# Optimization experiments

Hardware: AMD Instinct MI355X
Metric: run time of the kernel (lower is better)

Reference implementation:

```python
import jax, jax.numpy as jnp
import numpy as np

# Static config (matches init_kwargs: dim=64, ffn=2.66, kernel=3, smk=3, heads=2)
DIM = 64
NUM_HEADS = 2
KS = 3
SMK = 3
POOL = 7           # ContMix pools context to 7x7 -> 49 context tokens
HIDDEN = 172       # round_up(int(64*2.66), 4)
HIDDEN2 = 2 * HIDDEN
CTX_DW = HIDDEN2 // 4   # 86
CTX_DW12 = HIDDEN // 4  # 43
NK = SMK * SMK + KS * KS  # 18


def conv1x1(x, w):
    # x: [B,C,H,W], w: [O,C] -> [B,O,H,W]
    return jnp.einsum('bchw,oc->bohw', x, w)


def extract_patches(x, k):
    # x: [B,C,H,W] -> [B,C,k*k,H,W], zero ('same') padding, stride 1
    p = k // 2
    B, C, H, W = x.shape
    xp = jnp.pad(x, ((0, 0), (0, 0), (p, p), (p, p)))
    pats = [xp[:, :, i:i + H, j:j + W] for i in range(k) for j in range(k)]
    return jnp.stack(pats, axis=2)


def dyn_dw(x, attn, k, heads):
    # Dynamic depthwise mixing: per-pixel, per-head k*k kernel shared across
    # channels within a head. x: [B,C,H,W], attn: [B,g,HW,k*k]
    B, C, H, W = x.shape
    hd = C // heads
    pat = extract_patches(x, k).reshape(B, heads, hd, k * k, H * W)
    out = jnp.einsum('bgdkn,bgnk->bgdn', pat, attn)
    return out.reshape(B, C, H, W)


def contmix(x, ctx, wq, wk, wp, wpb, wo):
    # Content-aware dynamic depthwise-mixing (ContMix, OverLoCK-style).
    B, C, H, W = x.shape
    hd_qk = (C // 2) // NUM_HEADS
    scale = hd_qk ** -0.5
    # query from x, key from 7x7-pooled context
    q = conv1x1(x, wq) * scale                     # [B, C//2, H, W]
    ph, pw = H // POOL, W // POOL
    ctx_p = ctx.reshape(B, -1, POOL, ph, POOL, pw).mean(axis=(3, 5))  # [B,ctx,7,7]
    key = conv1x1(ctx_p, wk)                       # [B, C//2, 7, 7]
    q = q.reshape(B, NUM_HEADS, hd_qk, H * W)
    key = key.reshape(B, NUM_HEADS, hd_qk, POOL * POOL)
    w = jnp.einsum('bgcn,bgcl->bgnl', q, key)      # [B,g,HW,49]
    # project 49 context scores -> smk^2 + k^2 dynamic kernel taps (1x1 conv w/ bias)
    w = jnp.einsum('bgnl,ol->bgno', w, wp) + wpb   # [B,g,HW,18]
    a1 = jax.nn.softmax(w[..., :SMK * SMK], axis=-1)
    a2 = jax.nn.softmax(w[..., SMK * SMK:], axis=-1)
    # first channel half mixed with small kernel, second half with large kernel
    x1, x2 = jnp.split(x, 2, axis=1)
    y = jnp.concatenate([dyn_dw(x1, a1, SMK, NUM_HEADS),
                         dyn_dw(x2, a2, KS, NUM_HEADS)], axis=1)
    return conv1x1(y, wo)


def setup_inputs() -> dict:
    key = jax.random.key(0)
    ks = jax.random.split(key, 32)
    def w(i, o, c):
        return jax.random.normal(ks[i], (o, c), dtype=jnp.float32) / np.sqrt(c)
    inp = {
        'x': jax.random.normal(ks[0], (2, DIM, 112, 112), dtype=jnp.float32),
        'pin_w': w(1, HIDDEN2, DIM),
        'ctx_w': w(2, CTX_DW, HIDDEN2),
        'ctx1_w': w(3, CTX_DW12, HIDDEN),
        'ctx2_w': w(4, CTX_DW12, HIDDEN),
        'pout_w': w(5, DIM, HIDDEN),
        # ContMix on hidden_x2 (dim=344, ctx=86)
        'cm0_q': w(6, HIDDEN2 // 2, HIDDEN2),
        'cm0_k': w(7, HIDDEN2 // 2, CTX_DW),
        'cm0_p': w(8, NK, POOL * POOL),
        'cm0_pb': jnp.zeros((NK,), dtype=jnp.float32),
        'cm0_o': w(9, HIDDEN2, HIDDEN2),
        # ContMix on hidden (dim=172, ctx=43) -- branch 1
        'cm1_q': w(10, HIDDEN // 2, HIDDEN),
        'cm1_k': w(11, HIDDEN // 2, CTX_DW12),
        'cm1_p': w(12, NK, POOL * POOL),
        'cm1_pb': jnp.zeros((NK,), dtype=jnp.float32),
        'cm1_o': w(13, HIDDEN, HIDDEN),
        # ContMix on hidden -- branch 2
        'cm2_q': w(14, HIDDEN // 2, HIDDEN),
        'cm2_k': w(15, HIDDEN // 2, CTX_DW12),
        'cm2_p': w(16, NK, POOL * POOL),
        'cm2_pb': jnp.zeros((NK,), dtype=jnp.float32),
        'cm2_o': w(17, HIDDEN, HIDDEN),
    }
    return inp


def reference(x, pin_w, ctx_w, ctx1_w, ctx2_w, pout_w,
              cm0_q, cm0_k, cm0_p, cm0_pb, cm0_o,
              cm1_q, cm1_k, cm1_p, cm1_pb, cm1_o,
              cm2_q, cm2_k, cm2_p, cm2_pb, cm2_o):
    x_in = conv1x1(x, pin_w)                           # [B, 2*hidden, H, W]
    ctx_dw = conv1x1(x_in, ctx_w)                      # [B, ctx_dw, H, W]
    x_dw = contmix(x_in, ctx_dw, cm0_q, cm0_k, cm0_p, cm0_pb, cm0_o)
    x1, x2 = jnp.split(x_dw, 2, axis=1)                # each [B, hidden, H, W]
    ctx1 = conv1x1(x1, ctx1_w)
    ctx2 = conv1x1(x2, ctx2_w)
    x1p = jnp.tanh(contmix(x1, ctx1, cm1_q, cm1_k, cm1_p, cm1_pb, cm1_o)) + x1
    x2p = jnp.tanh(contmix(x2, ctx2, cm2_q, cm2_k, cm2_p, cm2_pb, cm2_o)) + x2
    out = conv1x1(x1p * x2p, pout_w)                   # [B, dim, H, W]
    return out
```

## Files before the change

kernel.cpp:

```cpp
#include <hip/hip_runtime.h>
#include <math.h>

#define HW 12544
#define W_IMG 112
#define B_SZ 2
#define RPAD 40

typedef __attribute__((ext_vector_type(8))) short s8v;
typedef __attribute__((ext_vector_type(4))) float f4v;

__device__ __forceinline__ void split_bf16(float x, unsigned short& h, unsigned short& l) {
    unsigned u  = __float_as_uint(x);
    unsigned hb = (u + 0x7FFFu + ((u >> 16) & 1u)) >> 16;
    float hf    = __uint_as_float(hb << 16);
    float r     = x - hf;
    unsigned ur = __float_as_uint(r);
    unsigned lb = (ur + 0x7FFFu + ((ur >> 16) & 1u)) >> 16;
    h = (unsigned short)hb; l = (unsigned short)lb;
}

struct WSplitArgs {
    const float* src[8];
    const float* src2[8];
    unsigned short* hi[8];
    unsigned short* lo[8];
    int O1[8]; int O2[8]; int O2B[8]; int K[8]; int Kp[8]; int MpKp[8];
    float scale2[8];
};

__global__ __launch_bounds__(256) void wsplit_k(WSplitArgs a) {
    const int ci  = blockIdx.y;
    const int idx = blockIdx.x * 256 + threadIdx.x;
    if (idx >= a.MpKp[ci]) return;
    const int Kp   = a.Kp[ci];
    const int mblk = idx / (32 * Kp);
    const int rem  = idx - mblk * 32 * Kp;
    const int kc   = rem >> 10;
    const int rem2 = rem & 1023;
    const int row  = rem2 >> 5, kk = rem2 & 31;
    const int o = mblk * 32 + row, k = kc * 32 + kk;
    float v = 0.f;
    if (k < a.K[ci]) {
        if (o < a.O1[ci])
            v = a.src[ci][(size_t)o * a.K[ci] + k];
        else if (o >= a.O2B[ci] && o - a.O2B[ci] < a.O2[ci])
            v = a.src2[ci][(size_t)(o - a.O2B[ci]) * a.K[ci] + k] * a.scale2[ci];
    }
    unsigned short h, l;
    split_bf16(v, h, l);
    a.hi[ci][idx] = h; a.lo[ci][idx] = l;
}

__global__ __launch_bounds__(256) void tsplit_k(
    const float* __restrict__ src, size_t bstride, int C, int KC,
    unsigned short* __restrict__ hi, unsigned short* __restrict__ lo)
{
    __shared__ __align__(16) float t[32][36];
    const int b   = blockIdx.z;
    const int hw0 = blockIdx.x * 32;
    const int kc  = blockIdx.y;
    const int c0  = kc * 32;
    const int tid = threadIdx.x;

    {
        const int cl = tid >> 3, hq = (tid & 7) * 4;
        const int c  = c0 + cl;
        float4 v = make_float4(0.f, 0.f, 0.f, 0.f);
        if (c < C)
            v = *(const float4*)(src + (size_t)b * bstride + (size_t)c * HW + hw0 + hq);
        *(float4*)&t[cl][hq] = v;
    }
    __syncthreads();

    const int hl = tid >> 3, cq = (tid & 7) * 4;
    float v0 = t[cq + 0][hl], v1 = t[cq + 1][hl], v2 = t[cq + 2][hl], v3 = t[cq + 3][hl];
    ushort4 h4, l4;
    split_bf16(v0, h4.x, l4.x);
    split_bf16(v1, h4.y, l4.y);
    split_bf16(v2, h4.z, l4.z);
    split_bf16(v3, h4.w, l4.w);
    const int ns = hw0 >> 8, r = (hw0 & 255) + hl;
    const size_t base = (((size_t)b * 49 + ns) * KC + kc) * 8192 + (size_t)r * 32 + cq;
    *(ushort4*)(hi + base) = h4;
    *(ushort4*)(lo + base) = l4;
}

template <int KP>
__global__ __launch_bounds__(256) void gemm_k(
    const unsigned short* __restrict__ bt_hi, const unsigned short* __restrict__ bt_lo,
    const unsigned short* __restrict__ w_hi,  const unsigned short* __restrict__ w_lo,
    int per_m,
    float* __restrict__ outA, int OA, size_t oa_bstride,
    float* __restrict__ outB, int OB, size_t ob_bstride, int obase,
    int mode, int Ovalid,
    const float* __restrict__ res, size_t res_bstride,
    const float* __restrict__ mul, size_t mul_bstride)
{
    constexpr int KC = KP / 32;
    __shared__ __align__(16) unsigned short Bh_s[256 * RPAD];
    __shared__ __align__(16) unsigned short Bl_s[256 * RPAD];
    __shared__ __align__(16) unsigned short Ah_s[32 * RPAD];
    __shared__ __align__(16) unsigned short Al_s[32 * RPAD];

    const int b   = blockIdx.y;
    const int bx  = blockIdx.x;
    const int xcd = bx & 7, t = bx >> 3;
    const int m   = t % per_m;
    const int ns  = (t / per_m) * 8 + xcd;
    if (ns >= 49) return;

    const int tid  = threadIdx.x;
    const int wv   = tid >> 6, lane = tid & 63;
    const int m16  = lane & 15, quad = lane >> 4;
    const int mbase = m * 32;
    const int nbase = ns * 256 + wv * 64;

    const unsigned short* Bh_g = bt_hi + ((size_t)b * 49 + ns) * KC * 8192;
    const unsigned short* Bl_g = bt_lo + ((size_t)b * 49 + ns) * KC * 8192;
    const unsigned short* Ah_g = w_hi + (size_t)m * KC * 1024;
    const unsigned short* Al_g = w_lo + (size_t)m * KC * 1024;

    const int srow = tid >> 2, schunk = tid & 3;
    const int arow = (tid & 127) >> 2, achunk = tid & 3;

    f4v acc0[4], acc1[4];
#pragma unroll
    for (int f = 0; f < 4; ++f) {
        acc0[f] = (f4v){0.f, 0.f, 0.f, 0.f};
        acc1[f] = (f4v){0.f, 0.f, 0.f, 0.f};
    }

    s8v rBh[4], rBl[4], rA;
#pragma unroll
    for (int j = 0; j < 4; ++j) {
        rBh[j] = *(const s8v*)(Bh_g + (size_t)(j * 256 + tid) * 8);
        rBl[j] = *(const s8v*)(Bl_g + (size_t)(j * 256 + tid) * 8);
    }
    rA = (tid < 128) ? *(const s8v*)(Ah_g + (size_t)tid * 8)
                     : *(const s8v*)(Al_g + (size_t)(tid - 128) * 8);
#pragma unroll
    for (int j = 0; j < 4; ++j) {
        *(s8v*)(Bh_s + (j * 64 + srow) * RPAD + schunk * 8) = rBh[j];
        *(s8v*)(Bl_s + (j * 64 + srow) * RPAD + schunk * 8) = rBl[j];
    }
    if (tid < 128) *(s8v*)(Ah_s + arow * RPAD + achunk * 8) = rA;
    else           *(s8v*)(Al_s + arow * RPAD + achunk * 8) = rA;
    __syncthreads();

#pragma unroll
    for (int kc = 0; kc < KC; ++kc) {
        if (kc + 1 < KC) {
            const size_t bo = (size_t)(kc + 1) * 8192;
            const size_t ao = (size_t)(kc + 1) * 1024;
#pragma unroll
            for (int j = 0; j < 4; ++j) {
                rBh[j] = *(const s8v*)(Bh_g + bo + (size_t)(j * 256 + tid) * 8);
                rBl[j] = *(const s8v*)(Bl_g + bo + (size_t)(j * 256 + tid) * 8);
            }
            rA = (tid < 128) ? *(const s8v*)(Ah_g + ao + (size_t)tid * 8)
                             : *(const s8v*)(Al_g + ao + (size_t)(tid - 128) * 8);
        }
        s8v ah0 = *(const s8v*)(Ah_s + m16 * RPAD + quad * 8);
        s8v al0 = *(const s8v*)(Al_s + m16 * RPAD + quad * 8);
        s8v ah1 = *(const s8v*)(Ah_s + (16 + m16) * RPAD + quad * 8);
        s8v al1 = *(const s8v*)(Al_s + (16 + m16) * RPAD + quad * 8);
#pragma unroll
        for (int f = 0; f < 4; ++f) {
            const int row = wv * 64 + f * 16 + m16;
            s8v bhf = *(const s8v*)(Bh_s + row * RPAD + quad * 8);
            s8v blf = *(const s8v*)(Bl_s + row * RPAD + quad * 8);
            acc0[f] = __builtin_amdgcn_mfma_f32_16x16x32_bf16(ah0, bhf, acc0[f], 0, 0, 0);
            acc0[f] = __builtin_amdgcn_mfma_f32_16x16x32_bf16(al0, bhf, acc0[f], 0, 0, 0);
            acc0[f] = __builtin_amdgcn_mfma_f32_16x16x32_bf16(ah0, blf, acc0[f], 0, 0, 0);
            acc1[f] = __builtin_amdgcn_mfma_f32_16x16x32_bf16(ah1, bhf, acc1[f], 0, 0, 0);
            acc1[f] = __builtin_amdgcn_mfma_f32_16x16x32_bf16(al1, bhf, acc1[f], 0, 0, 0);
            acc1[f] = __builtin_amdgcn_mfma_f32_16x16x32_bf16(ah1, blf, acc1[f], 0, 0, 0);
        }
        __syncthreads();
        if (kc + 1 < KC) {
#pragma unroll
            for (int j = 0; j < 4; ++j) {
                *(s8v*)(Bh_s + (j * 64 + srow) * RPAD + schunk * 8) = rBh[j];
                *(s8v*)(Bl_s + (j * 64 + srow) * RPAD + schunk * 8) = rBl[j];
            }
            if (tid < 128) *(s8v*)(Ah_s + arow * RPAD + achunk * 8) = rA;
            else           *(s8v*)(Al_s + arow * RPAD + achunk * 8) = rA;
            __syncthreads();
        }
    }

#pragma unroll
    for (int mp = 0; mp < 2; ++mp) {
#pragma unroll
        for (int f = 0; f < 4; ++f) {
            const int n = nbase + f * 16 + m16;
#pragma unroll
            for (int r = 0; r < 4; ++r) {
                const int o = mbase + mp * 16 + quad * 4 + r;
                float v = mp ? acc1[f][r] : acc0[f][r];
                if (mode == 2) {
                    if (o < Ovalid)
                        v = tanhf(v) + res[(size_t)b * res_bstride + (size_t)o * HW + n];
                } else if (mode == 3) {
                    if (o < Ovalid)
                        v = (tanhf(v) + res[(size_t)b * res_bstride + (size_t)o * HW + n])
                            * mul[(size_t)b * mul_bstride + (size_t)o * HW + n];
                }
                if (o < OA) {
                    outA[(size_t)b * oa_bstride + (size_t)o * HW + n] = v;
                } else if (o >= obase && o - obase < OB) {
                    outB[(size_t)b * ob_bstride + (size_t)(o - obase) * HW + n] = v;
                }
            }
        }
    }
}

__global__ __launch_bounds__(64) void pool_k(
    const float* __restrict__ ctx, float* __restrict__ pooled, int C)
{
    const int c = blockIdx.x, b = blockIdx.y, t = threadIdx.x;
    if (t >= 49) return;
    const int ph = t / 7, pw = t % 7;
    const float* src = ctx + ((size_t)b * C + c) * HW;
    float sum = 0.f;
    for (int i = 0; i < 16; ++i) {
        const float* row = src + (ph * 16 + i) * W_IMG + pw * 16;
        for (int j = 0; j < 16; ++j) sum += row[j];
    }
    pooled[((size_t)b * C + c) * 49 + t] = sum * (1.0f / 256.0f);
}

__global__ __launch_bounds__(64) void keygemm_k(
    const float* __restrict__ pooled, const float* __restrict__ wk,
    float* __restrict__ key, int K, int O)
{
    const int o = blockIdx.x, b = blockIdx.y, l = threadIdx.x;
    if (l >= 49) return;
    float s = 0.f;
    for (int c = 0; c < K; ++c)
        s += wk[(size_t)o * K + c] * pooled[((size_t)b * K + c) * 49 + l];
    key[((size_t)b * O + o) * 49 + l] = s;
}

__global__ __launch_bounds__(256) void attn_k(
    const float* __restrict__ q, const float* __restrict__ key,
    const float* __restrict__ wp, const float* __restrict__ pb,
    float* __restrict__ attn, int hd)
{
    __shared__ float klds[86 * 52];
    __shared__ float plds[18 * 52];
    __shared__ float pblds[18];

    const int b = blockIdx.z, g = blockIdx.y, tid = threadIdx.x;

    for (int idx = tid; idx < hd * 49; idx += 256) {
        int c = idx / 49, l = idx - c * 49;
        klds[c * 52 + l] = key[((size_t)(b * 2 + g) * hd + c) * 49 + l];
    }
    for (int idx = tid; idx < hd * 3; idx += 256) {
        int c = idx / 3;
        klds[c * 52 + 49 + (idx - c * 3)] = 0.f;
    }
    for (int idx = tid; idx < 18 * 49; idx += 256) {
        int o = idx / 49, l = idx - o * 49;
        plds[o * 52 + l] = wp[o * 49 + l];
    }
    for (int idx = tid; idx < 18 * 3; idx += 256) {
        int o = idx / 3;
        plds[o * 52 + 49 + (idx - o * 3)] = 0.f;
    }
    if (tid < 18) pblds[tid] = pb[tid];
    __syncthreads();

    const int hw = blockIdx.x * 256 + tid;

    float4 s[13];
#pragma unroll
    for (int t = 0; t < 13; ++t) s[t] = make_float4(0.f, 0.f, 0.f, 0.f);

    const float* qp = q + (size_t)(b * 2 + g) * hd * HW + hw;
    for (int c = 0; c < hd; ++c) {
        float qv = qp[(size_t)c * HW];
        const float4* kr = (const float4*)(klds + c * 52);
#pragma unroll
        for (int t = 0; t < 13; ++t) {
            float4 kv = kr[t];
            s[t].x += qv * kv.x; s[t].y += qv * kv.y;
            s[t].z += qv * kv.z; s[t].w += qv * kv.w;
        }
    }

    float e[18];
#pragma unroll
    for (int o = 0; o < 18; ++o) {
        const float4* pr = (const float4*)(plds + o * 52);
        float4 a = make_float4(0.f, 0.f, 0.f, 0.f);
#pragma unroll
        for (int t = 0; t < 13; ++t) {
            float4 pv = pr[t];
            a.x += s[t].x * pv.x; a.y += s[t].y * pv.y;
            a.z += s[t].z * pv.z; a.w += s[t].w * pv.w;
        }
        e[o] = pblds[o] + a.x + a.y + a.z + a.w;
    }

    float* outp = attn + (size_t)(b * 2 + g) * 18 * HW + hw;
#pragma unroll
    for (int half = 0; half < 2; ++half) {
        int base = half * 9;
        float m = e[base];
#pragma unroll
        for (int k = 1; k < 9; ++k) m = fmaxf(m, e[base + k]);
        float sum = 0.f, ex[9];
#pragma unroll
        for (int k = 0; k < 9; ++k) { ex[k] = expf(e[base + k] - m); sum += ex[k]; }
        float inv = 1.0f / sum;
#pragma unroll
        for (int k = 0; k < 9; ++k) outp[(size_t)(base + k) * HW] = ex[k] * inv;
    }
}

__global__ __launch_bounds__(256) void dyndw_k(
    const float* __restrict__ x, const float* __restrict__ attn,
    float* __restrict__ y, int C, int C_half, int hd, size_t x_bstride)
{
    const int b = blockIdx.z, c = blockIdx.y;
    const int hw = blockIdx.x * 256 + threadIdx.x;
    const int h = hw / W_IMG, w = hw - h * W_IMG;

    const int half = c / C_half;
    const int g = (c - half * C_half) / hd;

    const float* ap = attn + ((size_t)(b * 2 + g) * 18 + half * 9) * HW + hw;
    float a[9];
#pragma unroll
    for (int k = 0; k < 9; ++k) a[k] = ap[(size_t)k * HW];

    const float* xp = x + (size_t)b * x_bstride + (size_t)c * HW;
    float s = 0.f;
#pragma unroll
    for (int i = 0; i < 3; ++i) {
        int hh = h + i - 1;
#pragma unroll
        for (int j = 0; j < 3; ++j) {
            int ww = w + j - 1;
            float v = (hh >= 0 && hh < 112 && ww >= 0 && ww < 112)
                          ? xp[hh * W_IMG + ww] : 0.f;
            s += v * a[i * 3 + j];
        }
    }
    y[((size_t)b * C + c) * HW + hw] = s;
}

extern "C" void kernel_launch(void* const* d_in, const int* in_sizes, int n_in,
                              void* d_out, int out_size, void* d_ws, size_t ws_size,
                              hipStream_t stream) {
    const float* x      = (const float*)d_in[0];
    const float* pin_w  = (const float*)d_in[1];
    const float* ctx_w  = (const float*)d_in[2];
    const float* ctx1_w = (const float*)d_in[3];
    const float* ctx2_w = (const float*)d_in[4];
    const float* pout_w = (const float*)d_in[5];
    const float* cm0_q  = (const float*)d_in[6];
    const float* cm0_k  = (const float*)d_in[7];
    const float* cm0_p  = (const float*)d_in[8];
    const float* cm0_pb = (const float*)d_in[9];
    const float* cm0_o  = (const float*)d_in[10];
    const float* cm1_q  = (const float*)d_in[11];
    const float* cm1_k  = (const float*)d_in[12];
    const float* cm1_p  = (const float*)d_in[13];
    const float* cm1_pb = (const float*)d_in[14];
    const float* cm1_o  = (const float*)d_in[15];
    const float* cm2_q  = (const float*)d_in[16];
    const float* cm2_k  = (const float*)d_in[17];
    const float* cm2_p  = (const float*)d_in[18];
    const float* cm2_pb = (const float*)d_in[19];
    const float* cm2_o  = (const float*)d_in[20];
    float* out = (float*)d_out;

    float* ws = (float*)d_ws;
    float* x_in  = ws;
    float* x1p   = ws;
    float* y0    = ws + 8630272;
    float* y1    = ws + 8630272;
    float* prod  = ws + 8630272;
    float* y2    = ws + 12945408;
    float* x_dw  = ws + 17260544;
    float* ctxb  = ws + 25890816;
    float* ctx1  = ws + 28048384;
    float* ctx2  = ws + 29127168;
    float* q0    = ws + 30205952;
    float* q1    = ws + 30205952;
    float* q2    = ws + 32363520;
    float* attnb = ws + 34521088;
    float* pooled= ws + 35424256;
    float* keyb  = ws + 35432704;
    unsigned short* ub = (unsigned short*)(ws + 35449568);
    static const int WOFF[8] = {0, 45056, 247808, 518144, 579584, 641024, 714752, 788480};
    static const int WO1[8]  = {344, 86, 172, 43, 43, 172, 172, 64};
    static const int WO2[8]  = {0, 172, 172, 86, 86, 0, 0, 0};
    static const int O2B[8]  = {352, 86, 192, 43, 43, 192, 192, 64};
    static const int WK[8]   = {64, 344, 344, 172, 172, 172, 172, 172};
    static const int WKP[8]  = {64, 352, 352, 192, 192, 192, 192, 192};
    static const int WMP[8]  = {352, 288, 384, 160, 160, 192, 192, 64};
    unsigned short* xt_hi   = ub + 813056;
    unsigned short* xt_lo   = ub + 2418688;
    unsigned short* bigA_hi = ub + 4024320;
    unsigned short* bigA_lo = ub + 12855296;
    unsigned short* x1t_hi  = ub + 21686272;
    unsigned short* x1t_lo  = ub + 26503168;
    unsigned short* x2t_hi  = ub + 31320064;
    unsigned short* x2t_lo  = ub + 36136960;

    const float sc0 = 1.0f / sqrtf(86.0f);
    const float sc1 = 1.0f / sqrtf(43.0f);
    const size_t BS344 = (size_t)344 * HW, BS172 = (size_t)172 * HW,
                 BS86 = (size_t)86 * HW, BS64 = (size_t)64 * HW, BS43 = (size_t)43 * HW;

    WSplitArgs wa;
    const float* wsrc1[8] = {pin_w, ctx_w, cm0_o, ctx1_w, ctx2_w, cm1_o, cm2_o, pout_w};
    const float* wsrc2[8] = {nullptr, cm0_q, cm0_o + (size_t)172 * 344, cm1_q, cm2_q,
                             nullptr, nullptr, nullptr};
    const float wsc2[8]   = {1.f, sc0, 1.f, sc1, sc1, 1.f, 1.f, 1.f};
    for (int i = 0; i < 8; ++i) {
        wa.src[i] = wsrc1[i]; wa.src2[i] = wsrc2[i];
        wa.hi[i]  = ub + WOFF[i];
        wa.lo[i]  = ub + WOFF[i] + WMP[i] * WKP[i];
        wa.O1[i] = WO1[i]; wa.O2[i] = WO2[i]; wa.O2B[i] = O2B[i];
        wa.K[i] = WK[i]; wa.Kp[i] = WKP[i];
        wa.MpKp[i] = WMP[i] * WKP[i];
        wa.scale2[i] = wsc2[i];
    }
    wsplit_k<<<dim3(528, 8), 256, 0, stream>>>(wa);

#define WHI(CI) (ub + WOFF[CI])
#define WLO(CI) (ub + WOFF[CI] + WMP[CI] * WKP[CI])
#define GRID(CI) dim3((WMP[CI] / 32) * 56, B_SZ)

    tsplit_k<<<dim3(392, 2, B_SZ), 256, 0, stream>>>(x, BS64, 64, 2, xt_hi, xt_lo);
    gemm_k<64><<<GRID(0), 256, 0, stream>>>(
        xt_hi, xt_lo, WHI(0), WLO(0), WMP[0] / 32,
        x_in, 344, BS344, nullptr, 0, 0, 352, 0, 344,
        nullptr, 0, nullptr, 0);
    tsplit_k<<<dim3(392, 11, B_SZ), 256, 0, stream>>>(x_in, BS344, 344, 11, bigA_hi, bigA_lo);

    gemm_k<352><<<GRID(1), 256, 0, stream>>>(
        bigA_hi, bigA_lo, WHI(1), WLO(1), WMP[1] / 32,
        ctxb, 86, BS86, q0, 172, BS172, 86, 0, 258,
        nullptr, 0, nullptr, 0);
    pool_k<<<dim3(86, B_SZ), dim3(64), 0, stream>>>(ctxb, pooled, 86);
    keygemm_k<<<dim3(172, B_SZ), dim3(64), 0, stream>>>(pooled, cm0_k, keyb, 86, 172);
    attn_k<<<dim3(49, 2, B_SZ), dim3(256), 0, stream>>>(q0, keyb, cm0_p, cm0_pb, attnb, 86);
    dyndw_k<<<dim3(49, 344, B_SZ), dim3(256), 0, stream>>>(x_in, attnb, y0, 344, 172, 86, BS344);
    tsplit_k<<<dim3(392, 11, B_SZ), 256, 0, stream>>>(y0, BS344, 344, 11, bigA_hi, bigA_lo);
    gemm_k<352><<<GRID(2), 256, 0, stream>>>(
        bigA_hi, bigA_lo, WHI(2), WLO(2), WMP[2] / 32,
        x_dw, 172, BS344, x_dw + BS172, 172, BS344, 192, 0, 384,
        nullptr, 0, nullptr, 0);

    tsplit_k<<<dim3(392, 6, B_SZ), 256, 0, stream>>>(x_dw, BS344, 172, 6, x1t_hi, x1t_lo);
    tsplit_k<<<dim3(392, 6, B_SZ), 256, 0, stream>>>(x_dw + BS172, BS344, 172, 6, x2t_hi, x2t_lo);

    gemm_k<192><<<GRID(3), 256, 0, stream>>>(
        x1t_hi, x1t_lo, WHI(3), WLO(3), WMP[3] / 32,
        ctx1, 43, BS43, q1, 86, BS86, 43, 0, 129,
        nullptr, 0, nullptr, 0);
    pool_k<<<dim3(43, B_SZ), dim3(64), 0, stream>>>(ctx1, pooled, 43);
    keygemm_k<<<dim3(86, B_SZ), dim3(64), 0, stream>>>(pooled, cm1_k, keyb, 43, 86);
    attn_k<<<dim3(49, 2, B_SZ), dim3(256), 0, stream>>>(q1, keyb, cm1_p, cm1_pb, attnb, 43);
    dyndw_k<<<dim3(49, 172, B_SZ), dim3(256), 0, stream>>>(x_dw, attnb, y1, 172, 86, 43, BS344);
    tsplit_k<<<dim3(392, 6, B_SZ), 256, 0, stream>>>(y1, BS172, 172, 6, x1t_hi, x1t_lo);
    gemm_k<192><<<GRID(5), 256, 0, stream>>>(
        x1t_hi, x1t_lo, WHI(5), WLO(5), WMP[5] / 32,
        x1p, 172, BS172, nullptr, 0, 0, 192, 2, 172,
        x_dw, BS344, nullptr, 0);

    gemm_k<192><<<GRID(4), 256, 0, stream>>>(
        x2t_hi, x2t_lo, WHI(4), WLO(4), WMP[4] / 32,
        ctx2, 43, BS43, q2, 86, BS86, 43, 0, 129,
        nullptr, 0, nullptr, 0);
    pool_k<<<dim3(43, B_SZ), dim3(64), 0, stream>>>(ctx2, pooled, 43);
    keygemm_k<<<dim3(86, B_SZ), dim3(64), 0, stream>>>(pooled, cm2_k, keyb, 43, 86);
    attn_k<<<dim3(49, 2, B_SZ), dim3(256), 0, stream>>>(q2, keyb, cm2_p, cm2_pb, attnb, 43);
    dyndw_k<<<dim3(49, 172, B_SZ), dim3(256), 0, stream>>>(x_dw + BS172, attnb, y2, 172, 86, 43, BS344);
    tsplit_k<<<dim3(392, 6, B_SZ), 256, 0, stream>>>(y2, BS172, 172, 6, x2t_hi, x2t_lo);
    gemm_k<192><<<GRID(6), 256, 0, stream>>>(
        x2t_hi, x2t_lo, WHI(6), WLO(6), WMP[6] / 32,
        prod, 172, BS172, nullptr, 0, 0, 192, 3, 172,
        x_dw + BS172, BS344, x1p, BS172);

    tsplit_k<<<dim3(392, 6, B_SZ), 256, 0, stream>>>(prod, BS172, 172, 6, bigA_hi, bigA_lo);
    gemm_k<192><<<GRID(7), 256, 0, stream>>>(
        bigA_hi, bigA_lo, WHI(7), WLO(7), WMP[7] / 32,
        out, 64, BS64, nullptr, 0, 0, 64, 0, 64,
        nullptr, 0, nullptr, 0);

#undef WHI
#undef WLO
#undef GRID
}
```

Baseline: 584.2 us.

## Load GEMM operand fragments directly from global into registers, bypassing LDS

```diff
diff --git a/kernel.cpp b/kernel.cpp
--- a/kernel.cpp
+++ b/kernel.cpp
@@ -4,7 +4,6 @@
 #define HW 12544
 #define W_IMG 112
 #define B_SZ 2
-#define RPAD 40
 
 typedef __attribute__((ext_vector_type(8))) short s8v;
 typedef __attribute__((ext_vector_type(4))) float f4v;
@@ -97,10 +96,6 @@
     const float* __restrict__ mul, size_t mul_bstride)
 {
     constexpr int KC = KP / 32;
-    __shared__ __align__(16) unsigned short Bh_s[256 * RPAD];
-    __shared__ __align__(16) unsigned short Bl_s[256 * RPAD];
-    __shared__ __align__(16) unsigned short Ah_s[32 * RPAD];
-    __shared__ __align__(16) unsigned short Al_s[32 * RPAD];
 
     const int b   = blockIdx.y;
     const int bx  = blockIdx.x;
@@ -115,13 +110,12 @@
     const int mbase = m * 32;
     const int nbase = ns * 256 + wv * 64;
 
-    const unsigned short* Bh_g = bt_hi + ((size_t)b * 49 + ns) * KC * 8192;
-    const unsigned short* Bl_g = bt_lo + ((size_t)b * 49 + ns) * KC * 8192;
-    const unsigned short* Ah_g = w_hi + (size_t)m * KC * 1024;
-    const unsigned short* Al_g = w_lo + (size_t)m * KC * 1024;
-
-    const int srow = tid >> 2, schunk = tid & 3;
-    const int arow = (tid & 127) >> 2, achunk = tid & 3;
+    const unsigned short* Bh = bt_hi + ((size_t)b * 49 + ns) * KC * 8192;
+    const unsigned short* Bl = bt_lo + ((size_t)b * 49 + ns) * KC * 8192;
+    const unsigned short* Ah = w_hi + (size_t)m * KC * 1024;
+    const unsigned short* Al = w_lo + (size_t)m * KC * 1024;
+    const int boff = (wv * 64 + m16) * 32 + quad * 8;
+    const int aoff = m16 * 32 + quad * 8;
 
     f4v acc0[4], acc1[4];
 #pragma unroll
@@ -130,62 +124,46 @@
         acc1[f] = (f4v){0.f, 0.f, 0.f, 0.f};
     }
 
-    s8v rBh[4], rBl[4], rA;
-#pragma unroll
-    for (int j = 0; j < 4; ++j) {
-        rBh[j] = *(const s8v*)(Bh_g + (size_t)(j * 256 + tid) * 8);
-        rBl[j] = *(const s8v*)(Bl_g + (size_t)(j * 256 + tid) * 8);
-    }
-    rA = (tid < 128) ? *(const s8v*)(Ah_g + (size_t)tid * 8)
-                     : *(const s8v*)(Al_g + (size_t)(tid - 128) * 8);
-#pragma unroll
-    for (int j = 0; j < 4; ++j) {
-        *(s8v*)(Bh_s + (j * 64 + srow) * RPAD + schunk * 8) = rBh[j];
-        *(s8v*)(Bl_s + (j * 64 + srow) * RPAD + schunk * 8) = rBl[j];
-    }
-    if (tid < 128) *(s8v*)(Ah_s + arow * RPAD + achunk * 8) = rA;
-    else           *(s8v*)(Al_s + arow * RPAD + achunk * 8) = rA;
-    __syncthreads();
+    s8v cah0 = *(const s8v*)(Ah + aoff);
+    s8v cal0 = *(const s8v*)(Al + aoff);
+    s8v cah1 = *(const s8v*)(Ah + aoff + 512);
+    s8v cal1 = *(const s8v*)(Al + aoff + 512);
+    s8v cbh[4], cbl[4];
+#pragma unroll
+    for (int f = 0; f < 4; ++f) {
+        cbh[f] = *(const s8v*)(Bh + boff + f * 512);
+        cbl[f] = *(const s8v*)(Bl + boff + f * 512);
+    }
 
 #pragma unroll
     for (int kc = 0; kc < KC; ++kc) {
+        s8v nah0, nal0, nah1, nal1, nbh[4], nbl[4];
         if (kc + 1 < KC) {
-            const size_t bo = (size_t)(kc + 1) * 8192;
-            const size_t ao = (size_t)(kc + 1) * 1024;
-#pragma unroll
-            for (int j = 0; j < 4; ++j) {
-                rBh[j] = *(const s8v*)(Bh_g + bo + (size_t)(j * 256 + tid) * 8);
-                rBl[j] = *(const s8v*)(Bl_g + bo + (size_t)(j * 256 + tid) * 8);
+            const size_t ao = (size_t)(kc + 1) * 1024 + aoff;
+            const size_t bo = (size_t)(kc + 1) * 8192 + boff;
+            nah0 = *(const s8v*)(Ah + ao);
+            nal0 = *(const s8v*)(Al + ao);
+            nah1 = *(const s8v*)(Ah + ao + 512);
+            nal1 = *(const s8v*)(Al + ao + 512);
+#pragma unroll
+            for (int f = 0; f < 4; ++f) {
+                nbh[f] = *(const s8v*)(Bh + bo + f * 512);
+                nbl[f] = *(const s8v*)(Bl + bo + f * 512);
             }
-            rA = (tid < 128) ? *(const s8v*)(Ah_g + ao + (size_t)tid * 8)
-                             : *(const s8v*)(Al_g + ao + (size_t)(tid - 128) * 8);
-        }
-        s8v ah0 = *(const s8v*)(Ah_s + m16 * RPAD + quad * 8);
-        s8v al0 = *(const s8v*)(Al_s + m16 * RPAD + quad * 8);
-        s8v ah1 = *(const s8v*)(Ah_s + (16 + m16) * RPAD + quad * 8);
-        s8v al1 = *(const s8v*)(Al_s + (16 + m16) * RPAD + quad * 8);
+        }
 #pragma unroll
         for (int f = 0; f < 4; ++f) {
-            const int row = wv * 64 + f * 16 + m16;
-            s8v bhf = *(const s8v*)(Bh_s + row * RPAD + quad * 8);
-            s8v blf = *(const s8v*)(Bl_s + row * RPAD + quad * 8);
-            acc0[f] = __builtin_amdgcn_mfma_f32_16x16x32_bf16(ah0, bhf, acc0[f], 0, 0, 0);
-            acc0[f] = __builtin_amdgcn_mfma_f32_16x16x32_bf16(al0, bhf, acc0[f], 0, 0, 0);
-            acc0[f] = __builtin_amdgcn_mfma_f32_16x16x32_bf16(ah0, blf, acc0[f], 0, 0, 0);
-            acc1[f] = __builtin_amdgcn_mfma_f32_16x16x32_bf16(ah1, bhf, acc1[f], 0, 0, 0);
-            acc1[f] = __builtin_amdgcn_mfma_f32_16x16x32_bf16(al1, bhf, acc1[f], 0, 0, 0);
-            acc1[f] = __builtin_amdgcn_mfma_f32_16x16x32_bf16(ah1, blf, acc1[f], 0, 0, 0);
-        }
-        __syncthreads();
+            acc0[f] = __builtin_amdgcn_mfma_f32_16x16x32_bf16(cah0, cbh[f], acc0[f], 0, 0, 0);
+            acc0[f] = __builtin_amdgcn_mfma_f32_16x16x32_bf16(cal0, cbh[f], acc0[f], 0, 0, 0);
+            acc0[f] = __builtin_amdgcn_mfma_f32_16x16x32_bf16(cah0, cbl[f], acc0[f], 0, 0, 0);
+            acc1[f] = __builtin_amdgcn_mfma_f32_16x16x32_bf16(cah1, cbh[f], acc1[f], 0, 0, 0);
+            acc1[f] = __builtin_amdgcn_mfma_f32_16x16x32_bf16(cal1, cbh[f], acc1[f], 0, 0, 0);
+            acc1[f] = __builtin_amdgcn_mfma_f32_16x16x32_bf16(cah1, cbl[f], acc1[f], 0, 0, 0);
+        }
         if (kc + 1 < KC) {
-#pragma unroll
-            for (int j = 0; j < 4; ++j) {
-                *(s8v*)(Bh_s + (j * 64 + srow) * RPAD + schunk * 8) = rBh[j];
-                *(s8v*)(Bl_s + (j * 64 + srow) * RPAD + schunk * 8) = rBl[j];
-            }
-            if (tid < 128) *(s8v*)(Ah_s + arow * RPAD + achunk * 8) = rA;
-            else           *(s8v*)(Al_s + arow * RPAD + achunk * 8) = rA;
-            __syncthreads();
+            cah0 = nah0; cal0 = nal0; cah1 = nah1; cal1 = nal1;
+#pragma unroll
+            for (int f = 0; f < 4; ++f) { cbh[f] = nbh[f]; cbl[f] = nbl[f]; }
         }
     }
 
```

New measurement: 596.0 us. 2.0% more time.

## Reorder bf16 split tiles into k-quad-major layout for conflict-free LDS access

Applied to the files above, without the earlier changes.

```diff
diff --git a/kernel.cpp b/kernel.cpp
--- a/kernel.cpp
+++ b/kernel.cpp
@@ -4,7 +4,6 @@
 #define HW 12544
 #define W_IMG 112
 #define B_SZ 2
-#define RPAD 40
 
 typedef __attribute__((ext_vector_type(8))) short s8v;
 typedef __attribute__((ext_vector_type(4))) float f4v;
@@ -33,12 +32,15 @@
     const int idx = blockIdx.x * 256 + threadIdx.x;
     if (idx >= a.MpKp[ci]) return;
     const int Kp   = a.Kp[ci];
-    const int mblk = idx / (32 * Kp);
-    const int rem  = idx - mblk * 32 * Kp;
+    const int blk  = 32 * Kp;
+    const int mblk = idx / blk;
+    const int rem  = idx - mblk * blk;
     const int kc   = rem >> 10;
     const int rem2 = rem & 1023;
-    const int row  = rem2 >> 5, kk = rem2 & 31;
-    const int o = mblk * 32 + row, k = kc * 32 + kk;
+    const int kq   = rem2 >> 8;
+    const int row  = (rem2 >> 3) & 31;
+    const int j    = rem2 & 7;
+    const int o = mblk * 32 + row, k = kc * 32 + kq * 8 + j;
     float v = 0.f;
     if (k < a.K[ci]) {
         if (o < a.O1[ci])
@@ -80,7 +82,9 @@
     split_bf16(v2, h4.z, l4.z);
     split_bf16(v3, h4.w, l4.w);
     const int ns = hw0 >> 8, r = (hw0 & 255) + hl;
-    const size_t base = (((size_t)b * 49 + ns) * KC + kc) * 8192 + (size_t)r * 32 + cq;
+    const int kq = cq >> 3, j0 = cq & 7;
+    const size_t base = (((size_t)b * 49 + ns) * KC + kc) * 8192
+                        + (size_t)kq * 2048 + (size_t)r * 8 + j0;
     *(ushort4*)(hi + base) = h4;
     *(ushort4*)(lo + base) = l4;
 }
@@ -97,10 +101,10 @@
     const float* __restrict__ mul, size_t mul_bstride)
 {
     constexpr int KC = KP / 32;
-    __shared__ __align__(16) unsigned short Bh_s[256 * RPAD];
-    __shared__ __align__(16) unsigned short Bl_s[256 * RPAD];
-    __shared__ __align__(16) unsigned short Ah_s[32 * RPAD];
-    __shared__ __align__(16) unsigned short Al_s[32 * RPAD];
+    __shared__ __align__(16) unsigned short Bh_s[8192];
+    __shared__ __align__(16) unsigned short Bl_s[8192];
+    __shared__ __align__(16) unsigned short Ah_s[1024];
+    __shared__ __align__(16) unsigned short Al_s[1024];
 
     const int b   = blockIdx.y;
     const int bx  = blockIdx.x;
@@ -120,84 +124,79 @@
     const unsigned short* Ah_g = w_hi + (size_t)m * KC * 1024;
     const unsigned short* Al_g = w_lo + (size_t)m * KC * 1024;
 
-    const int srow = tid >> 2, schunk = tid & 3;
-    const int arow = (tid & 127) >> 2, achunk = tid & 3;
-
-    f4v acc0[4], acc1[4];
-#pragma unroll
-    for (int f = 0; f < 4; ++f) {
-        acc0[f] = (f4v){0.f, 0.f, 0.f, 0.f};
-        acc1[f] = (f4v){0.f, 0.f, 0.f, 0.f};
-    }
-
-    s8v rBh[4], rBl[4], rA;
+    f4v acc[2][4];
+#pragma unroll
+    for (int mt = 0; mt < 2; ++mt)
+#pragma unroll
+        for (int f = 0; f < 4; ++f) acc[mt][f] = (f4v){0.f, 0.f, 0.f, 0.f};
+
+    s8v rB[8], rA;
 #pragma unroll
     for (int j = 0; j < 4; ++j) {
-        rBh[j] = *(const s8v*)(Bh_g + (size_t)(j * 256 + tid) * 8);
-        rBl[j] = *(const s8v*)(Bl_g + (size_t)(j * 256 + tid) * 8);
+        rB[j]     = *(const s8v*)(Bh_g + (size_t)(j * 256 + tid) * 8);
+        rB[4 + j] = *(const s8v*)(Bl_g + (size_t)(j * 256 + tid) * 8);
     }
     rA = (tid < 128) ? *(const s8v*)(Ah_g + (size_t)tid * 8)
                      : *(const s8v*)(Al_g + (size_t)(tid - 128) * 8);
 #pragma unroll
     for (int j = 0; j < 4; ++j) {
-        *(s8v*)(Bh_s + (j * 64 + srow) * RPAD + schunk * 8) = rBh[j];
-        *(s8v*)(Bl_s + (j * 64 + srow) * RPAD + schunk * 8) = rBl[j];
-    }
-    if (tid < 128) *(s8v*)(Ah_s + arow * RPAD + achunk * 8) = rA;
-    else           *(s8v*)(Al_s + arow * RPAD + achunk * 8) = rA;
+        *(s8v*)(Bh_s + (j * 256 + tid) * 8) = rB[j];
+        *(s8v*)(Bl_s + (j * 256 + tid) * 8) = rB[4 + j];
+    }
+    if (tid < 128) *(s8v*)(Ah_s + tid * 8) = rA;
+    else           *(s8v*)(Al_s + (tid - 128) * 8) = rA;
     __syncthreads();
 
 #pragma unroll
     for (int kc = 0; kc < KC; ++kc) {
         if (kc + 1 < KC) {
-            const size_t bo = (size_t)(kc + 1) * 8192;
-            const size_t ao = (size_t)(kc + 1) * 1024;
+            const unsigned short* bh = Bh_g + (size_t)(kc + 1) * 8192;
+            const unsigned short* bl = Bl_g + (size_t)(kc + 1) * 8192;
 #pragma unroll
             for (int j = 0; j < 4; ++j) {
-                rBh[j] = *(const s8v*)(Bh_g + bo + (size_t)(j * 256 + tid) * 8);
-                rBl[j] = *(const s8v*)(Bl_g + bo + (size_t)(j * 256 + tid) * 8);
+                rB[j]     = *(const s8v*)(bh + (size_t)(j * 256 + tid) * 8);
+                rB[4 + j] = *(const s8v*)(bl + (size_t)(j * 256 + tid) * 8);
             }
-            rA = (tid < 128) ? *(const s8v*)(Ah_g + ao + (size_t)tid * 8)
-                             : *(const s8v*)(Al_g + ao + (size_t)(tid - 128) * 8);
-        }
-        s8v ah0 = *(const s8v*)(Ah_s + m16 * RPAD + quad * 8);
-        s8v al0 = *(const s8v*)(Al_s + m16 * RPAD + quad * 8);
-        s8v ah1 = *(const s8v*)(Ah_s + (16 + m16) * RPAD + quad * 8);
-        s8v al1 = *(const s8v*)(Al_s + (16 + m16) * RPAD + quad * 8);
-#pragma unroll
-        for (int f = 0; f < 4; ++f) {
-            const int row = wv * 64 + f * 16 + m16;
-            s8v bhf = *(const s8v*)(Bh_s + row * RPAD + quad * 8);
-            s8v blf = *(const s8v*)(Bl_s + row * RPAD + quad * 8);
-            acc0[f] = __builtin_amdgcn_mfma_f32_16x16x32_bf16(ah0, bhf, acc0[f], 0, 0, 0);
-            acc0[f] = __builtin_amdgcn_mfma_f32_16x16x32_bf16(al0, bhf, acc0[f], 0, 0, 0);
-            acc0[f] = __builtin_amdgcn_mfma_f32_16x16x32_bf16(ah0, blf, acc0[f], 0, 0, 0);
-            acc1[f] = __builtin_amdgcn_mfma_f32_16x16x32_bf16(ah1, bhf, acc1[f], 0, 0, 0);
-            acc1[f] = __builtin_amdgcn_mfma_f32_16x16x32_bf16(al1, bhf, acc1[f], 0, 0, 0);
-            acc1[f] = __builtin_amdgcn_mfma_f32_16x16x32_bf16(ah1, blf, acc1[f], 0, 0, 0);
+            rA = (tid < 128)
+                ? *(const s8v*)(Ah_g + (size_t)(kc + 1) * 1024 + (size_t)tid * 8)
+                : *(const s8v*)(Al_g + (size_t)(kc + 1) * 1024 + (size_t)(tid - 128) * 8);
+        }
+#pragma unroll
+        for (int mt = 0; mt < 2; ++mt) {
+            s8v ah = *(const s8v*)(Ah_s + (quad * 32 + mt * 16 + m16) * 8);
+            s8v al = *(const s8v*)(Al_s + (quad * 32 + mt * 16 + m16) * 8);
+#pragma unroll
+            for (int f = 0; f < 4; ++f) {
+                const int row = wv * 64 + f * 16 + m16;
+                s8v bh = *(const s8v*)(Bh_s + (quad * 256 + row) * 8);
+                s8v bl = *(const s8v*)(Bl_s + (quad * 256 + row) * 8);
+                acc[mt][f] = __builtin_amdgcn_mfma_f32_16x16x32_bf16(ah, bh, acc[mt][f], 0, 0, 0);
+                acc[mt][f] = __builtin_amdgcn_mfma_f32_16x16x32_bf16(al, bh, acc[mt][f], 0, 0, 0);
+                acc[mt][f] = __builtin_amdgcn_mfma_f32_16x16x32_bf16(ah, bl, acc[mt][f], 0, 0, 0);
+            }
         }
         __syncthreads();
         if (kc + 1 < KC) {
 #pragma unroll
             for (int j = 0; j < 4; ++j) {
-                *(s8v*)(Bh_s + (j * 64 + srow) * RPAD + schunk * 8) = rBh[j];
-                *(s8v*)(Bl_s + (j * 64 + srow) * RPAD + schunk * 8) = rBl[j];
+                *(s8v*)(Bh_s + (j * 256 + tid) * 8) = rB[j];
+                *(s8v*)(Bl_s + (j * 256 + tid) * 8) = rB[4 + j];
             }
-            if (tid < 128) *(s8v*)(Ah_s + arow * RPAD + achunk * 8) = rA;
-            else           *(s8v*)(Al_s + arow * RPAD + achunk * 8) = rA;
+            if (tid < 128) *(s8v*)(Ah_s + tid * 8) = rA;
+            else           *(s8v*)(Al_s + (tid - 128) * 8) = rA;
             __syncthreads();
         }
     }
 
 #pragma unroll
-    for (int mp = 0; mp < 2; ++mp) {
+    for (int mt = 0; mt < 2; ++mt) {
 #pragma unroll
         for (int f = 0; f < 4; ++f) {
             const int n = nbase + f * 16 + m16;
 #pragma unroll
             for (int r = 0; r < 4; ++r) {
-                const int o = mbase + mp * 16 + quad * 4 + r;
-                float v = mp ? acc1[f][r] : acc0[f][r];
+                const int o = mbase + mt * 16 + quad * 4 + r;
+                float v = acc[mt][f][r];
                 if (mode == 2) {
                     if (o < Ovalid)
                         v = tanhf(v) + res[(size_t)b * res_bstride + (size_t)o * HW + n];
```

Measured after the change: 555.1 us. -5.0%, faster.
